# Performance work log

Measured on AMD Instinct MI355X. Metric: run time of the kernel, lower is better.

## Reference

```python
import jax, jax.numpy as jnp
import numpy as np

ALPHA = 0.02
NEG = -9e15

def lrelu(x):
    return jnp.where(x >= 0, x, ALPHA * x)

def layer_norm(x, eps=1e-5):
    m = jnp.mean(x, axis=-1, keepdims=True)
    v = jnp.var(x, axis=-1, keepdims=True)
    return (x - m) * jax.lax.rsqrt(v + eps)

def setup_inputs() -> dict:
    key = jax.random.key(0)
    ks = jax.random.split(key, 10)
    B, N, F_IN, D = 8, 2048, 10, 128
    h = jax.random.normal(ks[0], (B, N, F_IN), jnp.float32)
    adj = jax.random.randint(ks[1], (B, N, N), 0, 2, jnp.int32)
    s = 0.1
    return {
        "h": h,
        "adj": adj,
        "W1": jax.random.normal(ks[2], (D, F_IN), jnp.float32) * s,
        "b1": jax.random.normal(ks[3], (D,), jnp.float32) * s,
        "Wg": jax.random.normal(ks[4], (D, D), jnp.float32) * s,
        "bg": jax.random.normal(ks[5], (D,), jnp.float32) * s,
        "a1": jax.random.normal(ks[6], (D,), jnp.float32) * s,
        "a2": jax.random.normal(ks[7], (D,), jnp.float32) * s,
        "W2": jax.random.normal(ks[8], (2, D), jnp.float32) * s,
        "b2": jax.random.normal(ks[9], (2,), jnp.float32) * s,
    }

def reference(h, adj, W1, b1, Wg, bg, a1, a2, W2, b2):
    # fc1 + layernorm + leakyrelu
    x = h @ W1.T + b1                      # [B,N,128]
    x = lrelu(layer_norm(x))
    # GAT layer
    Wh = x @ Wg.T + bg                     # [B,N,128]
    e1 = Wh @ a1                           # [B,N]
    e2 = Wh @ a2                           # [B,N]
    e = lrelu(e1[:, :, None] + e2[:, None, :])  # [B,N,N]
    e = jnp.where(adj != 0, e, NEG)
    attn = jax.nn.softmax(e, axis=2)
    hp = jnp.einsum('bij,bjd->bid', attn, Wh)    # [B,N,128]
    hp = lrelu(layer_norm(hp))
    # global max pool over nodes
    pooled = jnp.max(hp, axis=1)           # [B,128]
    out = pooled @ W2.T + b2               # [B,2]
    return jax.nn.log_softmax(out, axis=-1)
```

## Files before the change

kernel.cpp:

```cpp
#include <hip/hip_runtime.h>

#define B 8
#define N 2048
#define FIN 10
#define D 128
#define ALPHA 0.02f
#define BR 32
#define TI 32
#define JC 128
#define NCH (N / JC)
#define NBLK_ATTN ((N / TI) * B)

typedef short bf8 __attribute__((ext_vector_type(8)));
typedef float f32x4 __attribute__((ext_vector_type(4)));

__device__ __forceinline__ float lrelu(float x) { return x >= 0.f ? x : ALPHA * x; }

__device__ __forceinline__ short f2b(float f) {
    unsigned u = __float_as_uint(f);
    return (short)((u + 0x7fffu + ((u >> 16) & 1u)) >> 16);
}

__device__ __forceinline__ float b2f(short s) {
    return __uint_as_float(((unsigned)(unsigned short)s) << 16);
}

__device__ __forceinline__ unsigned enc_key(float v) {
    unsigned b = __float_as_uint(v);
    return (b & 0x80000000u) ? ~b : (b | 0x80000000u);
}
__device__ __forceinline__ float dec_key(unsigned k) {
    unsigned b = (k & 0x80000000u) ? (k & 0x7fffffffu) : ~k;
    return __uint_as_float(b);
}

__device__ __forceinline__ void dma16(const void* g, void* l) {
    __builtin_amdgcn_global_load_lds(
        (const __attribute__((address_space(1))) void*)g,
        (__attribute__((address_space(3))) void*)l, 16, 0, 0);
}
__device__ __forceinline__ void dma4(const void* g, void* l) {
    __builtin_amdgcn_global_load_lds(
        (const __attribute__((address_space(1))) void*)g,
        (__attribute__((address_space(3))) void*)l, 4, 0, 0);
}

__global__ __launch_bounds__(256) void k_proj(
    const float* __restrict__ h, const float* __restrict__ W1, const float* __restrict__ b1,
    const float* __restrict__ Wg, const float* __restrict__ bg,
    const float* __restrict__ a1, const float* __restrict__ a2,
    unsigned short* __restrict__ WhT, float* __restrict__ e1g, float* __restrict__ e2g,
    unsigned* __restrict__ pooled, unsigned* __restrict__ cnt)
{
    __shared__ __align__(16) short xep_lds[32 * 136];
    __shared__ __align__(16) short wg_lds[D * 136];
    __shared__ float W1_lds[D * 11];
    __shared__ float h_lds[BR * FIN];
    __shared__ float ep1[2][BR], ep2[2][BR];

    const int t = threadIdx.x;
    const int r0 = blockIdx.x * BR;
    const int bb = r0 >> 11;
    const int jloc = r0 & (N - 1);

    if (blockIdx.x < B && t < D) pooled[blockIdx.x * D + t] = 0u;
    if (blockIdx.x == 0 && t == 128) *cnt = 0u;

    for (int idx = t; idx < D * FIN; idx += 256)
        W1_lds[(idx / FIN) * 11 + (idx % FIN)] = W1[idx];
    for (int idx = t; idx < BR * FIN; idx += 256)
        h_lds[idx] = h[(size_t)r0 * FIN + idx];
    __syncthreads();

    {
        const int dr = t >> 4;
        const int j8 = t & 15;
        #pragma unroll
        for (int pass = 0; pass < 8; pass++) {
            int dd = pass * 16 + dr;
            float4 f0 = *(const float4*)&Wg[dd * D + j8 * 8];
            float4 f1 = *(const float4*)&Wg[dd * D + j8 * 8 + 4];
            bf8 v;
            v[0] = f2b(f0.x); v[1] = f2b(f0.y); v[2] = f2b(f0.z); v[3] = f2b(f0.w);
            v[4] = f2b(f1.x); v[5] = f2b(f1.y); v[6] = f2b(f1.z); v[7] = f2b(f1.w);
            *(bf8*)&wg_lds[dd * 136 + j8 * 8] = v;
        }
    }

    const int w = t >> 6, lane = t & 63;
    {
        float b1v0 = b1[lane], b1v1 = b1[lane + 64];
        for (int i = 0; i < 8; i++) {
            int r = w * 8 + i;
            float s0 = b1v0, s1 = b1v1;
            const float* hr = &h_lds[r * FIN];
            #pragma unroll
            for (int k = 0; k < FIN; k++) {
                float hv = hr[k];
                s0 += hv * W1_lds[lane * 11 + k];
                s1 += hv * W1_lds[(lane + 64) * 11 + k];
            }
            float sm = s0 + s1, sq = s0 * s0 + s1 * s1;
            #pragma unroll
            for (int m = 1; m <= 32; m <<= 1) { sm += __shfl_xor(sm, m); sq += __shfl_xor(sq, m); }
            float mean = sm * (1.f / D);
            float var  = sq * (1.f / D) - mean * mean;
            float rs = rsqrtf(var + 1e-5f);
            xep_lds[r * 136 + lane]      = f2b(lrelu((s0 - mean) * rs));
            xep_lds[r * 136 + lane + 64] = f2b(lrelu((s1 - mean) * rs));
        }
    }
    __syncthreads();

    const int l15 = lane & 15, q = lane >> 4;
    const int mw = w & 1, np = w >> 1;
    f32x4 acc[4];
    #pragma unroll
    for (int nt = 0; nt < 4; nt++)
        #pragma unroll
        for (int r = 0; r < 4; r++) acc[nt][r] = 0.f;

    #pragma unroll
    for (int ks = 0; ks < 4; ks++) {
        bf8 av = *(const bf8*)&xep_lds[(mw * 16 + l15) * 136 + ks * 32 + q * 8];
        #pragma unroll
        for (int nt = 0; nt < 4; nt++) {
            bf8 bv = *(const bf8*)&wg_lds[((np * 4 + nt) * 16 + l15) * 136 + ks * 32 + q * 8];
            acc[nt] = __builtin_amdgcn_mfma_f32_16x16x32_bf16(av, bv, acc[nt], 0, 0, 0);
        }
    }

    float e1p[4] = {0.f, 0.f, 0.f, 0.f}, e2p[4] = {0.f, 0.f, 0.f, 0.f};
    #pragma unroll
    for (int nt = 0; nt < 4; nt++) {
        int col = (np * 4 + nt) * 16 + l15;
        float bgv = bg[col], a1v = a1[col], a2v = a2[col];
        #pragma unroll
        for (int r = 0; r < 4; r++) {
            float v = acc[nt][r] + bgv;
            acc[nt][r] = v;
            e1p[r] += v * a1v;
            e2p[r] += v * a2v;
        }
    }
    #pragma unroll
    for (int m = 1; m <= 8; m <<= 1) {
        #pragma unroll
        for (int r = 0; r < 4; r++) { e1p[r] += __shfl_xor(e1p[r], m); e2p[r] += __shfl_xor(e2p[r], m); }
    }
    if (l15 == 0) {
        #pragma unroll
        for (int r = 0; r < 4; r++) {
            ep1[np][mw * 16 + q * 4 + r] = e1p[r];
            ep2[np][mw * 16 + q * 4 + r] = e2p[r];
        }
    }
    __syncthreads();
    if (t < BR) {
        e1g[r0 + t] = ep1[0][t] + ep1[1][t];
        e2g[r0 + t] = ep2[0][t] + ep2[1][t];
    }
    #pragma unroll
    for (int nt = 0; nt < 4; nt++) {
        int col = (np * 4 + nt) * 16 + l15;
        #pragma unroll
        for (int r = 0; r < 4; r++)
            xep_lds[col * 36 + mw * 16 + q * 4 + r] = f2b(acc[nt][r]);
    }
    __syncthreads();
    {
        const int col = t >> 1, jh = (t & 1) * 16;
        unsigned short* dst = WhT + ((size_t)(bb * D + col)) * N + jloc + jh;
        #pragma unroll
        for (int i2 = 0; i2 < 4; i2++)
            *(uint2*)(dst + i2 * 4) = *(const uint2*)&xep_lds[col * 36 + jh + i2 * 4];
    }
}

__global__ __launch_bounds__(512, 4) void k_attn(
    const int* __restrict__ adj, const unsigned short* __restrict__ WhT,
    const float* __restrict__ e1g, const float* __restrict__ e2g,
    unsigned* __restrict__ pooled, unsigned* __restrict__ cnt,
    const float* __restrict__ W2, const float* __restrict__ b2,
    float* __restrict__ out)
{
    __shared__ __align__(16) short whTL[D * JC];
    __shared__ __align__(16) int   adjL[2][TI * JC];
    __shared__ __align__(16) float e2L[2][JC];
    __shared__ __align__(16) short pT[TI * 136];
    __shared__ float statsp[4][TI][2];
    __shared__ float maxb[2][D];
    __shared__ float l_lds[TI];
    __shared__ int finalflag;

    const int t = threadIdx.x;
    const int b = blockIdx.y;
    const int i0 = blockIdx.x * TI;

    const int w = t >> 6, lane = t & 63;
    const int l15 = lane & 15, q = lane >> 4;
    const int mw = w & 1;
    const int np = w >> 1;

    const int sel = lane >> 4;
    const int c16 = lane & 15;
    const int row_a = 2 * w + ((sel >> 1) << 4) + (sel & 1);

    const float e1row = e1g[b * N + i0 + row_a];
    const unsigned short* WhTb = WhT + (size_t)b * D * N;
    const int* adjb = adj + ((size_t)b * N + i0) * N;
    const float* e2b = e2g + (size_t)b * N;

    f32x4 acc[2];
    #pragma unroll
    for (int nt = 0; nt < 2; nt++)
        #pragma unroll
        for (int r = 0; r < 4; r++) acc[nt][r] = 0.f;
    float ls = 0.f;

    auto stage_whT = [&](int jc) {
        #pragma unroll
        for (int p = 0; p < 4; p++) {
            int x = p * 8192 + w * 1024 + lane * 16;
            int rowx = x >> 8;
            int scol = (x & 255) ^ ((rowx & 7) << 4);
            dma16((const char*)WhTb + (size_t)rowx * (N * 2) + jc * (JC * 2) + scol,
                  (char*)whTL + x);
        }
    };
    auto stage_adj = [&](int jcn, int buf) {
        #pragma unroll
        for (int p = 0; p < 2; p++) {
            int y = p * 8192 + w * 1024 + lane * 16;
            int rowy = y >> 9;
            dma16((const char*)adjb + (size_t)rowy * (N * 4) + jcn * (JC * 4) + (y & 511),
                  (char*)&adjL[buf][0] + y);
        }
    };
    auto stage_e2 = [&](int jcn, int buf) {
        dma4((const char*)e2b + jcn * (JC * 4) + lane * 4,
             (char*)&e2L[buf][0] + lane * 4);
        dma4((const char*)e2b + jcn * (JC * 4) + 256 + lane * 4,
             (char*)&e2L[buf][0] + 256 + lane * 4);
    };

    stage_adj(0, 0);
    stage_e2(0, 0);

    for (int jc = 0; jc < NCH; jc++) {
        const int cb = jc & 1;
        const int jn = (jc + 1) & (NCH - 1);

        stage_whT(jc);
        stage_adj(jn, cb ^ 1);
        stage_e2(jn, cb ^ 1);

        asm volatile("s_waitcnt vmcnt(8)" ::: "memory");
        __builtin_amdgcn_sched_barrier(0);

        {
            const char* abase = (char*)&adjL[cb][0]
                + ((sel >> 1) << 13) + w * 1024 + ((sel & 1) << 9) + c16 * 32;
            int4 av0 = *(const int4*)abase;
            int4 av1 = *(const int4*)(abase + 16);
            const char* ebase = (char*)&e2L[cb][0] + c16 * 32;
            float4 ev0 = *(const float4*)ebase;
            float4 ev1 = *(const float4*)(ebase + 16);
            bf8 pv;
            pv[0] = f2b(av0.x ? __expf(lrelu(e1row + ev0.x)) : 0.f);
            pv[1] = f2b(av0.y ? __expf(lrelu(e1row + ev0.y)) : 0.f);
            pv[2] = f2b(av0.z ? __expf(lrelu(e1row + ev0.z)) : 0.f);
            pv[3] = f2b(av0.w ? __expf(lrelu(e1row + ev0.w)) : 0.f);
            pv[4] = f2b(av1.x ? __expf(lrelu(e1row + ev1.x)) : 0.f);
            pv[5] = f2b(av1.y ? __expf(lrelu(e1row + ev1.y)) : 0.f);
            pv[6] = f2b(av1.z ? __expf(lrelu(e1row + ev1.z)) : 0.f);
            pv[7] = f2b(av1.w ? __expf(lrelu(e1row + ev1.w)) : 0.f);
            ls += b2f(pv[0]) + b2f(pv[1]) + b2f(pv[2]) + b2f(pv[3])
                + b2f(pv[4]) + b2f(pv[5]) + b2f(pv[6]) + b2f(pv[7]);
            *(bf8*)&pT[row_a * 136 + c16 * 8] = pv;
        }

        asm volatile("s_waitcnt vmcnt(4) lgkmcnt(0)" ::: "memory");
        __builtin_amdgcn_sched_barrier(0);
        __builtin_amdgcn_s_barrier();

        __builtin_amdgcn_s_setprio(1);
        #pragma unroll
        for (int ks = 0; ks < 4; ks++) {
            bf8 av = *(const bf8*)&pT[(mw * 16 + l15) * 136 + ks * 32 + q * 8];
            #pragma unroll
            for (int nt = 0; nt < 2; nt++) {
                int rowb = (np * 2 + nt) * 16 + l15;
                const bf8* bp = (const bf8*)((char*)whTL + rowb * 256
                                  + (((ks * 64 + q * 16) ^ ((l15 & 7) << 4))));
                acc[nt] = __builtin_amdgcn_mfma_f32_16x16x32_bf16(av, *bp, acc[nt], 0, 0, 0);
            }
        }
        __builtin_amdgcn_s_setprio(0);

        asm volatile("s_waitcnt lgkmcnt(0)" ::: "memory");
        __builtin_amdgcn_sched_barrier(0);
        __builtin_amdgcn_s_barrier();
    }
    asm volatile("s_waitcnt vmcnt(0)" ::: "memory");

    #pragma unroll
    for (int m = 1; m <= 8; m <<= 1) ls += __shfl_xor(ls, m);
    if (c16 == 0) l_lds[row_a] = ls;
    __syncthreads();

    float smr[4] = {0.f, 0.f, 0.f, 0.f}, sqr[4] = {0.f, 0.f, 0.f, 0.f};
    #pragma unroll
    for (int r = 0; r < 4; r++) {
        float rinv = 1.f / l_lds[mw * 16 + q * 4 + r];
        #pragma unroll
        for (int nt = 0; nt < 2; nt++) {
            float v = acc[nt][r] * rinv;
            acc[nt][r] = v;
            smr[r] += v;
            sqr[r] += v * v;
        }
    }
    #pragma unroll
    for (int m = 1; m <= 8; m <<= 1) {
        #pragma unroll
        for (int r = 0; r < 4; r++) { smr[r] += __shfl_xor(smr[r], m); sqr[r] += __shfl_xor(sqr[r], m); }
    }
    if (l15 == 0) {
        #pragma unroll
        for (int r = 0; r < 4; r++) {
            statsp[np][mw * 16 + q * 4 + r][0] = smr[r];
            statsp[np][mw * 16 + q * 4 + r][1] = sqr[r];
        }
    }
    __syncthreads();

    float mx[2] = {-1e30f, -1e30f};
    #pragma unroll
    for (int r = 0; r < 4; r++) {
        int row = mw * 16 + q * 4 + r;
        float s0 = statsp[0][row][0] + statsp[1][row][0] + statsp[2][row][0] + statsp[3][row][0];
        float s1 = statsp[0][row][1] + statsp[1][row][1] + statsp[2][row][1] + statsp[3][row][1];
        float mean = s0 * (1.f / D);
        float var  = s1 * (1.f / D) - mean * mean;
        float rs = rsqrtf(var + 1e-5f);
        #pragma unroll
        for (int nt = 0; nt < 2; nt++) {
            float v = lrelu((acc[nt][r] - mean) * rs);
            mx[nt] = fmaxf(mx[nt], v);
        }
    }
    #pragma unroll
    for (int m = 16; m <= 32; m <<= 1) {
        #pragma unroll
        for (int nt = 0; nt < 2; nt++) mx[nt] = fmaxf(mx[nt], __shfl_xor(mx[nt], m));
    }
    if (q == 0) {
        #pragma unroll
        for (int nt = 0; nt < 2; nt++) maxb[mw][(np * 2 + nt) * 16 + l15] = mx[nt];
    }
    __syncthreads();
    if (t < D) {
        float v = fmaxf(maxb[0][t], maxb[1][t]);
        atomicMax(&pooled[b * D + t], enc_key(v));
    }
    __syncthreads();

    if (t == 0) {
        __threadfence();
        unsigned old = atomicAdd(cnt, 1u);
        finalflag = (old == NBLK_ATTN - 1) ? 1 : 0;
    }
    __syncthreads();
    if (finalflag && t < 256) {
        const int fb = t >> 5;
        const int fq = t & 31;
        float s0 = 0.f, s1 = 0.f;
        #pragma unroll
        for (int m = 0; m < 4; m++) {
            int dd = fq + 32 * m;
            unsigned key = __hip_atomic_load(&pooled[fb * D + dd], __ATOMIC_RELAXED,
                                             __HIP_MEMORY_SCOPE_AGENT);
            float v = dec_key(key);
            s0 += v * W2[dd];
            s1 += v * W2[D + dd];
        }
        #pragma unroll
        for (int m = 1; m <= 16; m <<= 1) { s0 += __shfl_xor(s0, m); s1 += __shfl_xor(s1, m); }
        if (fq == 0) {
            float o0 = s0 + b2[0], o1 = s1 + b2[1];
            float mxv = fmaxf(o0, o1);
            float ls2 = logf(__expf(o0 - mxv) + __expf(o1 - mxv));
            out[fb * 2 + 0] = o0 - mxv - ls2;
            out[fb * 2 + 1] = o1 - mxv - ls2;
        }
    }
}

extern "C" void kernel_launch(void* const* d_in, const int* in_sizes, int n_in,
                              void* d_out, int out_size, void* d_ws, size_t ws_size,
                              hipStream_t stream) {
    const float* h   = (const float*)d_in[0];
    const int*   adj = (const int*)d_in[1];
    const float* W1  = (const float*)d_in[2];
    const float* b1  = (const float*)d_in[3];
    const float* Wg  = (const float*)d_in[4];
    const float* bg  = (const float*)d_in[5];
    const float* a1  = (const float*)d_in[6];
    const float* a2  = (const float*)d_in[7];
    const float* W2  = (const float*)d_in[8];
    const float* b2  = (const float*)d_in[9];
    float* out = (float*)d_out;

    unsigned short* WhT = (unsigned short*)d_ws;
    float* e1g = (float*)((char*)d_ws + (size_t)B * D * N * 2);
    float* e2g = e1g + (size_t)B * N;
    unsigned* pooled = (unsigned*)(e2g + (size_t)B * N);
    unsigned* cnt = pooled + (size_t)B * D;

    k_proj<<<(B * N) / BR, 256, 0, stream>>>(h, W1, b1, Wg, bg, a1, a2,
                                             WhT, e1g, e2g, pooled, cnt);
    k_attn<<<dim3(N / TI, B), 512, 0, stream>>>(adj, WhT, e1g, e2g, pooled, cnt,
                                                W2, b2, out);
}
```

Baseline: 235.3 us.

## Bit-pack adjacency in projection kernel and triple-buffer WhT in attention loop

The projection kernel now reads each block's adjacency rows and packs them into 64-bit ballot masks, written to workspace. The attention kernel loads these compact masks and the whole e2 vector into LDS once, instead of streaming 32-bit adjacency and e2 per chunk. It also halves the chunk width and triple-buffers the WhT tiles with double-buffered P tiles, dropping one barrier per iteration. The aim is to cut the attention kernel's adjacency traffic and sync overhead, at the cost of an extra adjacency pass in k_proj and more loop iterations.

```diff
diff --git a/kernel.cpp b/kernel.cpp
--- a/kernel.cpp
+++ b/kernel.cpp
@@ -7,11 +7,12 @@
 #define ALPHA 0.02f
 #define BR 32
 #define TI 32
-#define JC 128
+#define JC 64
 #define NCH (N / JC)
 #define NBLK_ATTN ((N / TI) * B)
 
 typedef short bf8 __attribute__((ext_vector_type(8)));
+typedef short s4v __attribute__((ext_vector_type(4)));
 typedef float f32x4 __attribute__((ext_vector_type(4)));
 
 __device__ __forceinline__ float lrelu(float x) { return x >= 0.f ? x : ALPHA * x; }
@@ -39,17 +40,14 @@
         (const __attribute__((address_space(1))) void*)g,
         (__attribute__((address_space(3))) void*)l, 16, 0, 0);
 }
-__device__ __forceinline__ void dma4(const void* g, void* l) {
-    __builtin_amdgcn_global_load_lds(
-        (const __attribute__((address_space(1))) void*)g,
-        (__attribute__((address_space(3))) void*)l, 4, 0, 0);
-}
 
 __global__ __launch_bounds__(256) void k_proj(
-    const float* __restrict__ h, const float* __restrict__ W1, const float* __restrict__ b1,
+    const float* __restrict__ h, const int* __restrict__ adj,
+    const float* __restrict__ W1, const float* __restrict__ b1,
     const float* __restrict__ Wg, const float* __restrict__ bg,
     const float* __restrict__ a1, const float* __restrict__ a2,
     unsigned short* __restrict__ WhT, float* __restrict__ e1g, float* __restrict__ e2g,
+    unsigned long long* __restrict__ adjP,
     unsigned* __restrict__ pooled, unsigned* __restrict__ cnt)
 {
     __shared__ __align__(16) short xep_lds[32 * 136];
@@ -175,19 +173,32 @@
         for (int i2 = 0; i2 < 4; i2++)
             *(uint2*)(dst + i2 * 4) = *(const uint2*)&xep_lds[col * 36 + jh + i2 * 4];
     }
+
+    {
+        for (int rr = 0; rr < 8; rr++) {
+            const int row = w * 8 + rr;
+            const int* ar = adj + (size_t)(r0 + row) * N;
+            unsigned long long* dst = adjP + (size_t)(r0 + row) * (N / 64);
+            #pragma unroll 8
+            for (int w64 = 0; w64 < 32; w64++) {
+                unsigned long long m = __ballot(ar[w64 * 64 + lane] != 0);
+                if (lane == 0) dst[w64] = m;
+            }
+        }
+    }
 }
 
 __global__ __launch_bounds__(512, 4) void k_attn(
-    const int* __restrict__ adj, const unsigned short* __restrict__ WhT,
+    const unsigned long long* __restrict__ adjP, const unsigned short* __restrict__ WhT,
     const float* __restrict__ e1g, const float* __restrict__ e2g,
     unsigned* __restrict__ pooled, unsigned* __restrict__ cnt,
     const float* __restrict__ W2, const float* __restrict__ b2,
     float* __restrict__ out)
 {
-    __shared__ __align__(16) short whTL[D * JC];
-    __shared__ __align__(16) int   adjL[2][TI * JC];
-    __shared__ __align__(16) float e2L[2][JC];
-    __shared__ __align__(16) short pT[TI * 136];
+    __shared__ __align__(16) short whTL[3][D * JC];
+    __shared__ __align__(16) unsigned long long adjL[TI][32];
+    __shared__ __align__(16) float e2L[N];
+    __shared__ __align__(16) short pT[2][TI * 72];
     __shared__ float statsp[4][TI][2];
     __shared__ float maxb[2][D];
     __shared__ float l_lds[TI];
@@ -202,13 +213,12 @@
     const int mw = w & 1;
     const int np = w >> 1;
 
-    const int sel = lane >> 4;
-    const int c16 = lane & 15;
-    const int row_a = 2 * w + ((sel >> 1) << 4) + (sel & 1);
-
-    const float e1row = e1g[b * N + i0 + row_a];
+    const int ri = t >> 4;
+    const int c  = t & 15;
+
+    const float e1v = e1g[b * N + i0 + ri];
     const unsigned short* WhTb = WhT + (size_t)b * D * N;
-    const int* adjb = adj + ((size_t)b * N + i0) * N;
+    const unsigned long long* adjPb = adjP + (size_t)(b * N + i0) * (N / 64);
     const float* e2b = e2g + (size_t)b * N;
 
     f32x4 acc[2];
@@ -218,95 +228,68 @@
         for (int r = 0; r < 4; r++) acc[nt][r] = 0.f;
     float ls = 0.f;
 
-    auto stage_whT = [&](int jc) {
-        #pragma unroll
-        for (int p = 0; p < 4; p++) {
+    auto stage_whT = [&](int jcn, int buf) {
+        #pragma unroll
+        for (int p = 0; p < 2; p++) {
             int x = p * 8192 + w * 1024 + lane * 16;
-            int rowx = x >> 8;
-            int scol = (x & 255) ^ ((rowx & 7) << 4);
-            dma16((const char*)WhTb + (size_t)rowx * (N * 2) + jc * (JC * 2) + scol,
-                  (char*)whTL + x);
+            int rowx = x >> 7;
+            int scol = (x & 127) ^ ((rowx & 7) << 4);
+            dma16((const char*)WhTb + (size_t)rowx * (N * 2) + jcn * (JC * 2) + scol,
+                  (char*)&whTL[buf][0] + x);
         }
     };
-    auto stage_adj = [&](int jcn, int buf) {
-        #pragma unroll
-        for (int p = 0; p < 2; p++) {
-            int y = p * 8192 + w * 1024 + lane * 16;
-            int rowy = y >> 9;
-            dma16((const char*)adjb + (size_t)rowy * (N * 4) + jcn * (JC * 4) + (y & 511),
-                  (char*)&adjL[buf][0] + y);
-        }
-    };
-    auto stage_e2 = [&](int jcn, int buf) {
-        dma4((const char*)e2b + jcn * (JC * 4) + lane * 4,
-             (char*)&e2L[buf][0] + lane * 4);
-        dma4((const char*)e2b + jcn * (JC * 4) + 256 + lane * 4,
-             (char*)&e2L[buf][0] + 256 + lane * 4);
-    };
-
-    stage_adj(0, 0);
-    stage_e2(0, 0);
+
+    stage_whT(0, 0);
+    stage_whT(1, 1);
+    dma16((const char*)adjPb + w * 1024 + lane * 16, (char*)&adjL[0][0] + w * 1024 + lane * 16);
+    dma16((const char*)e2b + w * 1024 + lane * 16, (char*)&e2L[0] + w * 1024 + lane * 16);
+    asm volatile("s_waitcnt vmcnt(0)" ::: "memory");
+    __builtin_amdgcn_sched_barrier(0);
+    __builtin_amdgcn_s_barrier();
 
     for (int jc = 0; jc < NCH; jc++) {
         const int cb = jc & 1;
-        const int jn = (jc + 1) & (NCH - 1);
-
-        stage_whT(jc);
-        stage_adj(jn, cb ^ 1);
-        stage_e2(jn, cb ^ 1);
-
-        asm volatile("s_waitcnt vmcnt(8)" ::: "memory");
-        __builtin_amdgcn_sched_barrier(0);
 
         {
-            const char* abase = (char*)&adjL[cb][0]
-                + ((sel >> 1) << 13) + w * 1024 + ((sel & 1) << 9) + c16 * 32;
-            int4 av0 = *(const int4*)abase;
-            int4 av1 = *(const int4*)(abase + 16);
-            const char* ebase = (char*)&e2L[cb][0] + c16 * 32;
-            float4 ev0 = *(const float4*)ebase;
-            float4 ev1 = *(const float4*)(ebase + 16);
-            bf8 pv;
-            pv[0] = f2b(av0.x ? __expf(lrelu(e1row + ev0.x)) : 0.f);
-            pv[1] = f2b(av0.y ? __expf(lrelu(e1row + ev0.y)) : 0.f);
-            pv[2] = f2b(av0.z ? __expf(lrelu(e1row + ev0.z)) : 0.f);
-            pv[3] = f2b(av0.w ? __expf(lrelu(e1row + ev0.w)) : 0.f);
-            pv[4] = f2b(av1.x ? __expf(lrelu(e1row + ev1.x)) : 0.f);
-            pv[5] = f2b(av1.y ? __expf(lrelu(e1row + ev1.y)) : 0.f);
-            pv[6] = f2b(av1.z ? __expf(lrelu(e1row + ev1.z)) : 0.f);
-            pv[7] = f2b(av1.w ? __expf(lrelu(e1row + ev1.w)) : 0.f);
-            ls += b2f(pv[0]) + b2f(pv[1]) + b2f(pv[2]) + b2f(pv[3])
-                + b2f(pv[4]) + b2f(pv[5]) + b2f(pv[6]) + b2f(pv[7]);
-            *(bf8*)&pT[row_a * 136 + c16 * 8] = pv;
-        }
-
-        asm volatile("s_waitcnt vmcnt(4) lgkmcnt(0)" ::: "memory");
+            unsigned long long wbits = adjL[ri][jc];
+            unsigned nib = (unsigned)(wbits >> (c * 4)) & 0xFu;
+            float4 ev = *(const float4*)&e2L[jc * 64 + c * 4];
+            s4v pv;
+            pv[0] = f2b((nib & 1u) ? __expf(lrelu(e1v + ev.x)) : 0.f);
+            pv[1] = f2b((nib & 2u) ? __expf(lrelu(e1v + ev.y)) : 0.f);
+            pv[2] = f2b((nib & 4u) ? __expf(lrelu(e1v + ev.z)) : 0.f);
+            pv[3] = f2b((nib & 8u) ? __expf(lrelu(e1v + ev.w)) : 0.f);
+            ls += b2f(pv[0]) + b2f(pv[1]) + b2f(pv[2]) + b2f(pv[3]);
+            *(s4v*)&pT[cb][ri * 72 + c * 4] = pv;
+        }
+
+        asm volatile("s_waitcnt vmcnt(2) lgkmcnt(0)" ::: "memory");
         __builtin_amdgcn_sched_barrier(0);
         __builtin_amdgcn_s_barrier();
 
         __builtin_amdgcn_s_setprio(1);
-        #pragma unroll
-        for (int ks = 0; ks < 4; ks++) {
-            bf8 av = *(const bf8*)&pT[(mw * 16 + l15) * 136 + ks * 32 + q * 8];
+        const int rbuf = jc % 3;
+        #pragma unroll
+        for (int ks = 0; ks < 2; ks++) {
+            bf8 av = *(const bf8*)&pT[cb][(mw * 16 + l15) * 72 + ks * 32 + q * 8];
             #pragma unroll
             for (int nt = 0; nt < 2; nt++) {
-                int rowb = (np * 2 + nt) * 16 + l15;
-                const bf8* bp = (const bf8*)((char*)whTL + rowb * 256
-                                  + (((ks * 64 + q * 16) ^ ((l15 & 7) << 4))));
+                int brow = (np * 2 + nt) * 16 + l15;
+                const bf8* bp = (const bf8*)((const char*)&whTL[rbuf][0]
+                                 + brow * 128 + ((ks * 64 + q * 16) ^ ((brow & 7) << 4)));
                 acc[nt] = __builtin_amdgcn_mfma_f32_16x16x32_bf16(av, *bp, acc[nt], 0, 0, 0);
             }
         }
         __builtin_amdgcn_s_setprio(0);
 
-        asm volatile("s_waitcnt lgkmcnt(0)" ::: "memory");
-        __builtin_amdgcn_sched_barrier(0);
-        __builtin_amdgcn_s_barrier();
-    }
-    asm volatile("s_waitcnt vmcnt(0)" ::: "memory");
+        if (jc + 2 < NCH) stage_whT(jc + 2, (jc + 2) % 3);
+    }
+
+    asm volatile("s_waitcnt vmcnt(0) lgkmcnt(0)" ::: "memory");
 
     #pragma unroll
     for (int m = 1; m <= 8; m <<= 1) ls += __shfl_xor(ls, m);
-    if (c16 == 0) l_lds[row_a] = ls;
+    if ((lane & 15) == 0) l_lds[ri] = ls;
     __syncthreads();
 
     float smr[4] = {0.f, 0.f, 0.f, 0.f}, sqr[4] = {0.f, 0.f, 0.f, 0.f};
@@ -415,11 +398,12 @@
     unsigned short* WhT = (unsigned short*)d_ws;
     float* e1g = (float*)((char*)d_ws + (size_t)B * D * N * 2);
     float* e2g = e1g + (size_t)B * N;
-    unsigned* pooled = (unsigned*)(e2g + (size_t)B * N);
+    unsigned long long* adjP = (unsigned long long*)(e2g + (size_t)B * N);
+    unsigned* pooled = (unsigned*)(adjP + (size_t)B * N * (N / 64));
     unsigned* cnt = pooled + (size_t)B * D;
 
-    k_proj<<<(B * N) / BR, 256, 0, stream>>>(h, W1, b1, Wg, bg, a1, a2,
-                                             WhT, e1g, e2g, pooled, cnt);
-    k_attn<<<dim3(N / TI, B), 512, 0, stream>>>(adj, WhT, e1g, e2g, pooled, cnt,
+    k_proj<<<(B * N) / BR, 256, 0, stream>>>(h, adj, W1, b1, Wg, bg, a1, a2,
+                                             WhT, e1g, e2g, adjP, pooled, cnt);
+    k_attn<<<dim3(N / TI, B), 512, 0, stream>>>(adjP, WhT, e1g, e2g, pooled, cnt,
                                                 W2, b2, out);
 }
```

After: 352.8 us. 49.9% more time.
